# Performance work log

Measured on AMD Instinct MI355X. Metric: run time of the kernel, lower is better.

## Reference

```python
import jax, jax.numpy as jnp
import numpy as np

B, P, L = 8, 196, 80
DIM1, DIM2, ATT = 2048, 300, 1024


def setup_inputs() -> dict:
    key = jax.random.key(0)
    ks = jax.random.split(key, 8)
    s1 = 1.0 / np.sqrt(DIM1)
    s2 = 1.0 / np.sqrt(DIM2)
    sa = 1.0 / np.sqrt(ATT)
    return {
        "x1": jax.random.normal(ks[0], (B, P, DIM1), jnp.float32),
        "x2": jax.random.normal(ks[1], (B, L, DIM2), jnp.float32),
        "W1": jax.random.uniform(ks[2], (ATT, DIM1), jnp.float32, -s1, s1),
        "W2": jax.random.uniform(ks[3], (ATT, DIM2), jnp.float32, -s2, s2),
        "Wh": jax.random.uniform(ks[4], (ATT, ATT), jnp.float32, -sa, sa),
        "bh": jax.random.uniform(ks[5], (ATT,), jnp.float32, -sa, sa),
        "wt": jax.random.uniform(ks[6], (ATT,), jnp.float32, -sa, sa),
        "bt": jax.random.uniform(ks[7], (), jnp.float32, -sa, sa),
    }


def reference(x1, x2, W1, W2, Wh, bh, wt, bt):
    # project: p1 (B,P,A), p2 (B,L,A)
    p1 = jnp.einsum("bpd,ad->bpa", x1, W1)
    p2 = jnp.einsum("bld,ad->bla", x2, W2)
    # broadcast bilinear + tanh: (B,L,P,A)
    h = jnp.tanh(p1[:, None, :, :] * p2[:, :, None, :])
    # hidden linear then target linear (rank-1 on last dim)
    t = jnp.einsum("blpa,ca->blpc", h, Wh) + bh
    alpha = jnp.einsum("blpc,c->blp", t, wt) + bt  # (B,L,P)
    return alpha
```

## Files before the change

kernel.cpp:

```cpp
#include <hip/hip_runtime.h>
#include <hip/hip_bf16.h>

static constexpr int kB   = 8;
static constexpr int kP   = 196;
static constexpr int kL   = 80;
static constexpr int kD1  = 2048;
static constexpr int kD2  = 300;
static constexpr int kD2p = 320;
static constexpr int kATT = 1024;
static constexpr int kM   = kB * kP;
static constexpr int kR2  = kB * kL;
static constexpr int kOut = kB * kL * kP;
static constexpr int kASplit = 16;
static constexpr int kAChunk = kATT / kASplit;
static constexpr int kLPer   = 5;
static constexpr int kVPart  = 16;
static constexpr int kPadA   = kAChunk + 4;

static constexpr float kTanhScale = 2.8853900817779268f;

__device__ __forceinline__ unsigned short f2bf(float x) {
    union { float f; unsigned int u; } c; c.f = x;
    unsigned int r = c.u + 0x7fffu + ((c.u >> 16) & 1u);
    return (unsigned short)(r >> 16);
}

typedef __attribute__((ext_vector_type(8))) short  bf16x8;
typedef __attribute__((ext_vector_type(4))) float  f32x4;

__device__ __forceinline__ void load_lds16(const void* g, void* l) {
    __builtin_amdgcn_global_load_lds(
        (const __attribute__((address_space(1))) void*)g,
        (__attribute__((address_space(3))) void*)l, 16, 0, 0);
}

static constexpr int kN4a = kM * kD1 / 4;
static constexpr int kN4b = kATT * kD1 / 4;
static constexpr int kN1  = kR2 * kD2p;
static constexpr int kN2  = kATT * kD2p;
static constexpr int kCastBlocks =
    (kN4a + kN4b + kN1 + kN2 + 255) / 256;

__global__ __launch_bounds__(256) void prep_kernel(
        const float* __restrict__ x1, unsigned short* __restrict__ x1b,
        const float* __restrict__ W1, unsigned short* __restrict__ W1b,
        const float* __restrict__ x2, unsigned short* __restrict__ x2b,
        const float* __restrict__ W2, unsigned short* __restrict__ W2b,
        const float* __restrict__ Wh, const float* __restrict__ wt,
        const float* __restrict__ bh, const float* __restrict__ bt,
        float* __restrict__ vpart, float* __restrict__ beta) {
    if (blockIdx.x >= kCastBlocks) {
        int bid = blockIdx.x - kCastBlocks;
        int ax  = bid & 3;
        int cg  = bid >> 2;
        int c0  = cg * 64;
        int a   = ax * 256 + threadIdx.x;
        float acc = 0.0f;
        #pragma unroll 8
        for (int c = c0; c < c0 + 64; ++c)
            acc = fmaf(wt[c], Wh[(size_t)c * kATT + a], acc);
        vpart[(size_t)cg * kATT + a] = acc;
        if (bid == 0 && threadIdx.x < 64) {
            float pb = 0.0f;
            #pragma unroll 4
            for (int c = threadIdx.x; c < kATT; c += 64)
                pb = fmaf(wt[c], bh[c], pb);
            #pragma unroll
            for (int off = 32; off > 0; off >>= 1)
                pb += __shfl_down(pb, off, 64);
            if (threadIdx.x == 0) beta[0] = pb + bt[0];
        }
        return;
    }
    int i = blockIdx.x * 256 + threadIdx.x;
    if (i < kN4a) {
        float4 f = ((const float4*)x1)[i];
        ushort4 o = { f2bf(f.x), f2bf(f.y), f2bf(f.z), f2bf(f.w) };
        ((ushort4*)x1b)[i] = o;
    } else if ((i -= kN4a) < kN4b) {
        float4 f = ((const float4*)W1)[i];
        ushort4 o = { f2bf(f.x), f2bf(f.y), f2bf(f.z), f2bf(f.w) };
        ((ushort4*)W1b)[i] = o;
    } else if ((i -= kN4b) < kN1) {
        int r = i / kD2p, c = i - r * kD2p;
        x2b[i] = (c < kD2) ? f2bf(x2[(size_t)r * kD2 + c]) : (unsigned short)0;
    } else if ((i -= kN1) < kN2) {
        int r = i / kD2p, c = i - r * kD2p;
        W2b[i] = (c < kD2) ? f2bf(W2[(size_t)r * kD2 + c]) : (unsigned short)0;
    }
}

static constexpr int kP1Mt      = (kM + 127) / 128;
static constexpr int kP1Blocks  = kP1Mt * (kATT / 128) * 2;
static constexpr int kP2Blocks  = (kR2 / 64) * (kATT / 64);
static constexpr int kInitBlocks = (kOut + 255) / 256;
static constexpr int kVBlocks   = kATT / 256;
static constexpr int kKHalf     = kD1 / 2;

__global__ __launch_bounds__(256) void gemm_all_kernel(
        const unsigned short* __restrict__ x2b, const unsigned short* __restrict__ W2b,
        float* __restrict__ p2w,
        const unsigned short* __restrict__ x1b, const unsigned short* __restrict__ W1b,
        float* __restrict__ p1a, float* __restrict__ p1b,
        const float* __restrict__ beta, float* __restrict__ outp,
        const float* __restrict__ vpart, float* __restrict__ v) {
    __shared__ unsigned short As2[2][128 * 64];
    __shared__ unsigned short Bs2[2][128 * 64];

    const int bid  = blockIdx.x;
    const int tid  = threadIdx.x;
    const int lane = tid & 63;
    const int wv   = tid >> 6;

    if (bid >= kP1Blocks + kP2Blocks) {
        int r = bid - kP1Blocks - kP2Blocks;
        if (r < kInitBlocks) {
            int i = r * 256 + tid;
            if (i < kOut) outp[i] = beta[0];
        } else {
            int a = (r - kInitBlocks) * 256 + tid;
            float s = 0.0f;
            #pragma unroll
            for (int g = 0; g < kVPart; ++g)
                s += vpart[(size_t)g * kATT + a];
            v[a] = s;
        }
        return;
    }

    if (bid < kP1Blocks) {
        const int l  = bid;
        const int ks = l & 1;
        const int t  = l >> 1;
        const int mx = t % kP1Mt, nx = t / kP1Mt;
        const int m0 = mx * 128, n0 = nx * 128;
        const int kBeg = ks * kKHalf;

        const int srow = tid >> 3;
        const int kx   = ((tid & 7) ^ (srow & 7)) * 8;
        int ar[4], br[4];
        #pragma unroll
        for (int q = 0; q < 4; ++q) {
            ar[q] = min(m0 + srow + q * 32, kM - 1);
            br[q] = n0 + srow + q * 32;
        }
        const int wr = (wv >> 1) * 64;
        const int wc = (wv & 1) * 64;

        f32x4 acc[4][4] = {};

        #pragma unroll
        for (int q = 0; q < 4; ++q) {
            load_lds16(x1b + (size_t)ar[q] * kD1 + kBeg + kx,
                       (char*)As2[0] + (tid + q * 256) * 16);
            load_lds16(W1b + (size_t)br[q] * kD1 + kBeg + kx,
                       (char*)Bs2[0] + (tid + q * 256) * 16);
        }
        __syncthreads();

        int buf = 0;
        for (int k0 = 0; k0 < kKHalf; k0 += 64) {
            if (k0 + 64 < kKHalf) {
                const int kp = kBeg + k0 + 64;
                #pragma unroll
                for (int q = 0; q < 4; ++q) {
                    load_lds16(x1b + (size_t)ar[q] * kD1 + kp + kx,
                               (char*)As2[buf ^ 1] + (tid + q * 256) * 16);
                    load_lds16(W1b + (size_t)br[q] * kD1 + kp + kx,
                               (char*)Bs2[buf ^ 1] + (tid + q * 256) * 16);
                }
            }
            const char* Ap = (const char*)As2[buf];
            const char* Bp = (const char*)Bs2[buf];
            #pragma unroll
            for (int kk = 0; kk < 2; ++kk) {
                bf16x8 af[4], bf[4];
                #pragma unroll
                for (int i = 0; i < 4; ++i) {
                    int r   = wr + i * 16 + (lane & 15);
                    int col = (kk * 64 + (lane >> 4) * 16) ^ ((r & 7) << 4);
                    af[i] = *(const bf16x8*)(Ap + r * 128 + col);
                }
                #pragma unroll
                for (int j = 0; j < 4; ++j) {
                    int r   = wc + j * 16 + (lane & 15);
                    int col = (kk * 64 + (lane >> 4) * 16) ^ ((r & 7) << 4);
                    bf[j] = *(const bf16x8*)(Bp + r * 128 + col);
                }
                #pragma unroll
                for (int i = 0; i < 4; ++i)
                    #pragma unroll
                    for (int j = 0; j < 4; ++j)
                        acc[i][j] = __builtin_amdgcn_mfma_f32_16x16x32_bf16(
                                        af[i], bf[j], acc[i][j], 0, 0, 0);
            }
            __syncthreads();
            buf ^= 1;
        }

        float* Co = ks ? p1b : p1a;
        #pragma unroll
        for (int i = 0; i < 4; ++i)
            #pragma unroll
            for (int j = 0; j < 4; ++j)
                #pragma unroll
                for (int r = 0; r < 4; ++r) {
                    int m = m0 + wr + i * 16 + (lane >> 4) * 4 + r;
                    int n = n0 + wc + j * 16 + (lane & 15);
                    if (m < kM) Co[(size_t)m * kATT + n] = kTanhScale * acc[i][j][r];
                }
        return;
    }

    {
        const int l  = bid - kP1Blocks;
        const int mx = l % (kR2 / 64), nx = l / (kR2 / 64);
        const int m0 = mx * 64, n0 = nx * 64;
        unsigned short* As = As2[0];
        unsigned short* Bs = Bs2[0];

        const int mh = (wv >> 1) * 32;
        const int nh = (wv & 1) * 32;
        const int row0 = tid >> 3;
        const int kx   = ((tid & 7) ^ (row0 & 7)) * 8;
        const int ar0 = min(m0 + row0, kR2 - 1), ar1 = min(m0 + row0 + 32, kR2 - 1);
        const int br0 = n0 + row0,               br1 = n0 + row0 + 32;

        f32x4 acc[2][2] = {};
        for (int k0 = 0; k0 < kD2p; k0 += 64) {
            load_lds16(x2b + (size_t)ar0 * kD2p + k0 + kx, (char*)As + tid * 16);
            load_lds16(x2b + (size_t)ar1 * kD2p + k0 + kx, (char*)As + (tid + 256) * 16);
            load_lds16(W2b + (size_t)br0 * kD2p + k0 + kx, (char*)Bs + tid * 16);
            load_lds16(W2b + (size_t)br1 * kD2p + k0 + kx, (char*)Bs + (tid + 256) * 16);
            __syncthreads();

            #pragma unroll
            for (int kk = 0; kk < 2; ++kk) {
                bf16x8 af[2], bf[2];
                #pragma unroll
                for (int i = 0; i < 2; ++i) {
                    int r   = mh + i * 16 + (lane & 15);
                    int col = (kk * 64 + (lane >> 4) * 16) ^ ((r & 7) << 4);
                    af[i] = *(const bf16x8*)((const char*)As + r * 128 + col);
                }
                #pragma unroll
                for (int j = 0; j < 2; ++j) {
                    int r   = nh + j * 16 + (lane & 15);
                    int col = (kk * 64 + (lane >> 4) * 16) ^ ((r & 7) << 4);
                    bf[j] = *(const bf16x8*)((const char*)Bs + r * 128 + col);
                }
                #pragma unroll
                for (int i = 0; i < 2; ++i)
                    #pragma unroll
                    for (int j = 0; j < 2; ++j)
                        acc[i][j] = __builtin_amdgcn_mfma_f32_16x16x32_bf16(
                                        af[i], bf[j], acc[i][j], 0, 0, 0);
            }
            __syncthreads();
        }

        #pragma unroll
        for (int i = 0; i < 2; ++i)
            #pragma unroll
            for (int j = 0; j < 2; ++j)
                #pragma unroll
                for (int r = 0; r < 4; ++r) {
                    int m = m0 + mh + i * 16 + (lane >> 4) * 4 + r;
                    int n = n0 + nh + j * 16 + (lane & 15);
                    if (m < kR2) p2w[(size_t)m * kATT + n] = acc[i][j][r];
                }
    }
}

__global__ __launch_bounds__(256) void alpha_kernel(
        const float* __restrict__ p1A, const float* __restrict__ p1B,
        const float* __restrict__ p2,
        const float* __restrict__ v, float* __restrict__ outp) {
    __shared__ float us[16][kPadA];
    __shared__ float wsm[kL][kPadA];
    __shared__ float vs[kAChunk];
    __shared__ float sred;
    const int b     = blockIdx.y;
    const int as    = blockIdx.z;
    const int aBase = as * kAChunk;
    const int p0    = blockIdx.x * 16;
    const int tid   = threadIdx.x;
    const int tp    = tid & 15;
    const int lg    = tid >> 4;

    {
        int row = tid >> 4, col = tid & 15;
        int gp  = min(p0 + row, kP - 1);
        size_t base = ((size_t)(b * kP + gp)) * kATT + aBase + col * 4;
        float4 ua = *(const float4*)(p1A + base);
        float4 ub = *(const float4*)(p1B + base);
        float4 s  = { ua.x + ub.x, ua.y + ub.y, ua.z + ub.z, ua.w + ub.w };
        *(float4*)&us[row][col * 4] = s;
    }
    #pragma unroll
    for (int q = 0; q < 5; ++q) {
        int idx = q * 256 + tid;
        int row = idx >> 4, col = idx & 15;
        size_t base = ((size_t)(b * kL + row)) * kATT + aBase + col * 4;
        *(float4*)&wsm[row][col * 4] = *(const float4*)(p2 + base);
    }
    if (tid < kAChunk) vs[tid] = v[aBase + tid];
    __syncthreads();

    if (tid < 64) {
        float s = vs[tid];
        #pragma unroll
        for (int off = 32; off > 0; off >>= 1)
            s += __shfl_down(s, off, 64);
        if (tid == 0) sred = s;
    }
    __syncthreads();
    const float sumV = sred;

    float acc[kLPer] = {};
    #pragma unroll 4
    for (int a4 = 0; a4 < kAChunk / 4; ++a4) {
        float4 u  = *(const float4*)&us[tp][a4 * 4];
        float4 vv = *(const float4*)&vs[a4 * 4];
        #pragma unroll
        for (int j = 0; j < kLPer; ++j) {
            float4 w = *(const float4*)&wsm[lg * kLPer + j][a4 * 4];
            acc[j] = fmaf(vv.x, __builtin_amdgcn_rcpf(__builtin_amdgcn_exp2f(u.x * w.x) + 1.0f), acc[j]);
            acc[j] = fmaf(vv.y, __builtin_amdgcn_rcpf(__builtin_amdgcn_exp2f(u.y * w.y) + 1.0f), acc[j]);
            acc[j] = fmaf(vv.z, __builtin_amdgcn_rcpf(__builtin_amdgcn_exp2f(u.z * w.z) + 1.0f), acc[j]);
            acc[j] = fmaf(vv.w, __builtin_amdgcn_rcpf(__builtin_amdgcn_exp2f(u.w * w.w) + 1.0f), acc[j]);
        }
    }
    const int p = p0 + tp;
    if (p < kP) {
        float* po = outp + ((size_t)b * kL + lg * kLPer) * kP + p;
        #pragma unroll
        for (int j = 0; j < kLPer; ++j)
            atomicAdd(&po[(size_t)j * kP], sumV - 2.0f * acc[j]);
    }
}

extern "C" void kernel_launch(void* const* d_in, const int* in_sizes, int n_in,
                              void* d_out, int out_size, void* d_ws, size_t ws_size,
                              hipStream_t stream) {
    const float* x1 = (const float*)d_in[0];
    const float* x2 = (const float*)d_in[1];
    const float* W1 = (const float*)d_in[2];
    const float* W2 = (const float*)d_in[3];
    const float* Wh = (const float*)d_in[4];
    const float* bh = (const float*)d_in[5];
    const float* wt = (const float*)d_in[6];
    const float* bt = (const float*)d_in[7];
    float* out = (float*)d_out;

    float* ws    = (float*)d_ws;
    float* v     = ws;
    float* vpart = ws + 1024;
    float* beta  = vpart + (size_t)kVPart * kATT;
    float* p2w   = beta + 64;
    float* p1a   = p2w + (size_t)kR2 * kATT;
    float* p1b   = p1a + (size_t)kM * kATT;
    unsigned short* x1b = (unsigned short*)(p1b + (size_t)kM * kATT);
    unsigned short* W1b = x1b + (size_t)kM * kD1;
    unsigned short* x2b = W1b + (size_t)kATT * kD1;
    unsigned short* W2b = x2b + (size_t)kR2 * kD2p;

    prep_kernel<<<dim3(kCastBlocks + 64), 256, 0, stream>>>(
        x1, x1b, W1, W1b, x2, x2b, W2, W2b, Wh, wt, bh, bt, vpart, beta);
    gemm_all_kernel<<<dim3(kP1Blocks + kP2Blocks + kInitBlocks + kVBlocks),
                     256, 0, stream>>>(
        x2b, W2b, p2w, x1b, W1b, p1a, p1b, beta, out, vpart, v);
    alpha_kernel<<<dim3((kP + 15) / 16, kB, kASplit), 256, 0, stream>>>(
        p1a, p1b, p2w, v, out);
}
```

Measured before the change: 136.6 us.

## Enlarge alpha kernel tile to 32 p-rows and loop two A-chunks per block

The alpha kernel now handles 32 positions per block instead of 16, so each loaded p2 tile is reused across twice as many p rows. Each block also walks two 64-wide attention chunks serially, halving the A-split and so halving the atomicAdd traffic to the output. This cuts redundant p2 loads and atomic contention. The cost is a grid that shrinks from 13x8x16 to 7x8x8 blocks, extra register pressure from the doubled accumulators, and a block size fixed at 32 positions that leaves more idle rows in the last tile.

```diff
diff --git a/kernel.cpp b/kernel.cpp
--- a/kernel.cpp
+++ b/kernel.cpp
@@ -11,11 +11,12 @@
 static constexpr int kM   = kB * kP;
 static constexpr int kR2  = kB * kL;
 static constexpr int kOut = kB * kL * kP;
-static constexpr int kASplit = 16;
-static constexpr int kAChunk = kATT / kASplit;
+static constexpr int kAChunk = 64;
+static constexpr int kASplit = 8;
 static constexpr int kLPer   = 5;
 static constexpr int kVPart  = 16;
 static constexpr int kPadA   = kAChunk + 4;
+static constexpr int kPTile  = 32;
 
 static constexpr float kTanhScale = 2.8853900817779268f;
 
@@ -32,6 +33,10 @@
     __builtin_amdgcn_global_load_lds(
         (const __attribute__((address_space(1))) void*)g,
         (__attribute__((address_space(3))) void*)l, 16, 0, 0);
+}
+
+__device__ __forceinline__ float sigl(float uw) {
+    return __builtin_amdgcn_rcpf(__builtin_amdgcn_exp2f(uw) + 1.0f);
 }
 
 static constexpr int kN4a = kM * kD1 / 4;
@@ -276,67 +281,83 @@
         const float* __restrict__ p1A, const float* __restrict__ p1B,
         const float* __restrict__ p2,
         const float* __restrict__ v, float* __restrict__ outp) {
-    __shared__ float us[16][kPadA];
+    __shared__ float us[kPTile][kPadA];
     __shared__ float wsm[kL][kPadA];
     __shared__ float vs[kAChunk];
     __shared__ float sred;
-    const int b     = blockIdx.y;
-    const int as    = blockIdx.z;
-    const int aBase = as * kAChunk;
-    const int p0    = blockIdx.x * 16;
-    const int tid   = threadIdx.x;
-    const int tp    = tid & 15;
-    const int lg    = tid >> 4;
-
-    {
-        int row = tid >> 4, col = tid & 15;
-        int gp  = min(p0 + row, kP - 1);
-        size_t base = ((size_t)(b * kP + gp)) * kATT + aBase + col * 4;
-        float4 ua = *(const float4*)(p1A + base);
-        float4 ub = *(const float4*)(p1B + base);
-        float4 s  = { ua.x + ub.x, ua.y + ub.y, ua.z + ub.z, ua.w + ub.w };
-        *(float4*)&us[row][col * 4] = s;
-    }
+    const int b   = blockIdx.y;
+    const int as  = blockIdx.z;
+    const int p0  = blockIdx.x * kPTile;
+    const int tid = threadIdx.x;
+    const int tp  = tid & 15;
+    const int lg  = tid >> 4;
+
+    float acc[2][kLPer] = {};
+    float sumV = 0.0f;
+
+    for (int ac = 0; ac < 2; ++ac) {
+        const int aBase = (as * 2 + ac) * kAChunk;
+
+        #pragma unroll
+        for (int q = 0; q < 2; ++q) {
+            int idx = q * 256 + tid;
+            int row = idx >> 4, col = idx & 15;
+            int gp  = min(p0 + row, kP - 1);
+            size_t base = ((size_t)(b * kP + gp)) * kATT + aBase + col * 4;
+            float4 ua = *(const float4*)(p1A + base);
+            float4 ub = *(const float4*)(p1B + base);
+            float4 s  = { ua.x + ub.x, ua.y + ub.y, ua.z + ub.z, ua.w + ub.w };
+            *(float4*)&us[row][col * 4] = s;
+        }
+        #pragma unroll
+        for (int q = 0; q < 5; ++q) {
+            int idx = q * 256 + tid;
+            int row = idx >> 4, col = idx & 15;
+            size_t base = ((size_t)(b * kL + row)) * kATT + aBase + col * 4;
+            *(float4*)&wsm[row][col * 4] = *(const float4*)(p2 + base);
+        }
+        if (tid < kAChunk) vs[tid] = v[aBase + tid];
+        __syncthreads();
+
+        if (tid < 64) {
+            float s = vs[tid];
+            #pragma unroll
+            for (int off = 32; off > 0; off >>= 1)
+                s += __shfl_down(s, off, 64);
+            if (tid == 0) sred = s;
+        }
+
+        #pragma unroll 4
+        for (int a4 = 0; a4 < kAChunk / 4; ++a4) {
+            float4 u0 = *(const float4*)&us[tp][a4 * 4];
+            float4 u1 = *(const float4*)&us[tp + 16][a4 * 4];
+            float4 vv = *(const float4*)&vs[a4 * 4];
+            #pragma unroll
+            for (int j = 0; j < kLPer; ++j) {
+                float4 w = *(const float4*)&wsm[lg * kLPer + j][a4 * 4];
+                acc[0][j] = fmaf(vv.x, sigl(u0.x * w.x), acc[0][j]);
+                acc[0][j] = fmaf(vv.y, sigl(u0.y * w.y), acc[0][j]);
+                acc[0][j] = fmaf(vv.z, sigl(u0.z * w.z), acc[0][j]);
+                acc[0][j] = fmaf(vv.w, sigl(u0.w * w.w), acc[0][j]);
+                acc[1][j] = fmaf(vv.x, sigl(u1.x * w.x), acc[1][j]);
+                acc[1][j] = fmaf(vv.y, sigl(u1.y * w.y), acc[1][j]);
+                acc[1][j] = fmaf(vv.z, sigl(u1.z * w.z), acc[1][j]);
+                acc[1][j] = fmaf(vv.w, sigl(u1.w * w.w), acc[1][j]);
+            }
+        }
+        __syncthreads();
+        sumV += sred;
+    }
+
     #pragma unroll
-    for (int q = 0; q < 5; ++q) {
-        int idx = q * 256 + tid;
-        int row = idx >> 4, col = idx & 15;
-        size_t base = ((size_t)(b * kL + row)) * kATT + aBase + col * 4;
-        *(float4*)&wsm[row][col * 4] = *(const float4*)(p2 + base);
-    }
-    if (tid < kAChunk) vs[tid] = v[aBase + tid];
-    __syncthreads();
-
-    if (tid < 64) {
-        float s = vs[tid];
-        #pragma unroll
-        for (int off = 32; off > 0; off >>= 1)
-            s += __shfl_down(s, off, 64);
-        if (tid == 0) sred = s;
-    }
-    __syncthreads();
-    const float sumV = sred;
-
-    float acc[kLPer] = {};
-    #pragma unroll 4
-    for (int a4 = 0; a4 < kAChunk / 4; ++a4) {
-        float4 u  = *(const float4*)&us[tp][a4 * 4];
-        float4 vv = *(const float4*)&vs[a4 * 4];
-        #pragma unroll
-        for (int j = 0; j < kLPer; ++j) {
-            float4 w = *(const float4*)&wsm[lg * kLPer + j][a4 * 4];
-            acc[j] = fmaf(vv.x, __builtin_amdgcn_rcpf(__builtin_amdgcn_exp2f(u.x * w.x) + 1.0f), acc[j]);
-            acc[j] = fmaf(vv.y, __builtin_amdgcn_rcpf(__builtin_amdgcn_exp2f(u.y * w.y) + 1.0f), acc[j]);
-            acc[j] = fmaf(vv.z, __builtin_amdgcn_rcpf(__builtin_amdgcn_exp2f(u.z * w.z) + 1.0f), acc[j]);
-            acc[j] = fmaf(vv.w, __builtin_amdgcn_rcpf(__builtin_amdgcn_exp2f(u.w * w.w) + 1.0f), acc[j]);
-        }
-    }
-    const int p = p0 + tp;
-    if (p < kP) {
-        float* po = outp + ((size_t)b * kL + lg * kLPer) * kP + p;
-        #pragma unroll
-        for (int j = 0; j < kLPer; ++j)
-            atomicAdd(&po[(size_t)j * kP], sumV - 2.0f * acc[j]);
+    for (int pi = 0; pi < 2; ++pi) {
+        int p = p0 + tp + pi * 16;
+        if (p < kP) {
+            float* po = outp + ((size_t)b * kL + lg * kLPer) * kP + p;
+            #pragma unroll
+            for (int j = 0; j < kLPer; ++j)
+                atomicAdd(&po[(size_t)j * kP], sumV - 2.0f * acc[pi][j]);
+        }
     }
 }
 
@@ -370,6 +391,6 @@
     gemm_all_kernel<<<dim3(kP1Blocks + kP2Blocks + kInitBlocks + kVBlocks),
                      256, 0, stream>>>(
         x2b, W2b, p2w, x1b, W1b, p1a, p1b, beta, out, vpart, v);
-    alpha_kernel<<<dim3((kP + 15) / 16, kB, kASplit), 256, 0, stream>>>(
+    alpha_kernel<<<dim3((kP + kPTile - 1) / kPTile, kB, kASplit), 256, 0, stream>>>(
         p1a, p1b, p2w, v, out);
 }
```

New measurement: 144.2 us. 1.06x slower.
